# Optimization experiments

Measured on AMD Instinct MI355X. Metric: run time of the kernel, lower is better.

The kernel has to match this reference:

```python
import jax, jax.numpy as jnp
import numpy as np

B, IN, H, OUT, E = 8192, 1024, 4096, 1024, 8
HG = H // 2  # gating hidden

def setup_inputs() -> dict:
    key = jax.random.key(0)
    ks = jax.random.split(key, 9)
    s_in = 1.0 / np.sqrt(IN)
    s_h = 1.0 / np.sqrt(H)
    s_hg = 1.0 / np.sqrt(HG)
    return {
        "x": jax.random.normal(ks[0], (B, IN), jnp.float32),
        # gating MLP: Linear(IN,HG) -> ReLU -> Linear(HG,E) -> softmax
        "gw1": jax.random.uniform(ks[1], (IN, HG), jnp.float32, -s_in, s_in),
        "gb1": jax.random.uniform(ks[2], (HG,), jnp.float32, -s_in, s_in),
        "gw2": jax.random.uniform(ks[3], (HG, E), jnp.float32, -s_hg, s_hg),
        "gb2": jax.random.uniform(ks[4], (E,), jnp.float32, -s_hg, s_hg),
        # experts: E x (Linear(IN,H) -> ReLU -> Linear(H,OUT))
        "ew1": jax.random.uniform(ks[5], (E, IN, H), jnp.float32, -s_in, s_in),
        "eb1": jax.random.uniform(ks[6], (E, H), jnp.float32, -s_in, s_in),
        "ew2": jax.random.uniform(ks[7], (E, H, OUT), jnp.float32, -s_h, s_h),
        "eb2": jax.random.uniform(ks[8], (E, OUT), jnp.float32, -s_h, s_h),
    }

def reference(x, gw1, gb1, gw2, gb2, ew1, eb1, ew2, eb2):
    # Gating network (dropout is a no-op in eval)
    gh = jax.nn.relu(x @ gw1 + gb1)                       # [B, HG]
    gates = jax.nn.softmax(gh @ gw2 + gb2, axis=1)        # [B, E]
    # All experts run on the full batch
    h = jax.nn.relu(jnp.einsum('bi,eih->beh', x, ew1) + eb1[None])  # [B, E, H]
    eo = jnp.einsum('beh,eho->beo', h, ew2) + eb2[None]             # [B, E, OUT]
    # Gate-weighted combine: (stacked * gates[...,None]).sum(dim=1)
    combined = jnp.einsum('beo,be->bo', eo, gates)        # [B, OUT]
    return combined
```

## Files before the change

kernel.cpp:

```cpp
#include <hip/hip_runtime.h>


#define DI __device__ __forceinline__

typedef _Float16 f16;
typedef _Float16 f16x8 __attribute__((ext_vector_type(8)));
typedef float f32x4 __attribute__((ext_vector_type(4)));

constexpr int BSZ  = 8192;
constexpr int IND  = 1024;
constexpr int HID  = 4096;
constexpr int OUTD = 1024;
constexpr int NE   = 8;
constexpr int HGD  = 2048;

__global__ __launch_bounds__(256) void conv_f32_f16_kernel(
    const float* __restrict__ in, f16* __restrict__ out)
{
    size_t i = ((size_t)blockIdx.x * 256 + threadIdx.x) * 8;
    const float4* p = (const float4*)(in + i);
    float4 a = p[0], b = p[1];
    f16x8 v = {(f16)a.x, (f16)a.y, (f16)a.z, (f16)a.w,
               (f16)b.x, (f16)b.y, (f16)b.z, (f16)b.w};
    *(f16x8*)(out + i) = v;
}

__global__ __launch_bounds__(256) void transpose_f32_f16_kernel(
    const float* __restrict__ W, f16* __restrict__ Wt, int K, int N,
    int ldo, size_t zstride, int kostep)
{
    const int z = blockIdx.z;
    W += (size_t)z * K * N;
    f16* base = Wt + (size_t)z * zstride + (size_t)z * kostep;
    __shared__ float t[64][65];
    int n0 = blockIdx.x * 64, k0 = blockIdx.y * 64;
    int tx = threadIdx.x & 63, ty = threadIdx.x >> 6;
#pragma unroll
    for (int i = 0; i < 16; i++) {
        int k = i * 4 + ty;
        t[k][tx] = W[(size_t)(k0 + k) * N + n0 + tx];
    }
    __syncthreads();
#pragma unroll
    for (int i = 0; i < 16; i++) {
        int n = i * 4 + ty;
        base[(size_t)(n0 + n) * ldo + k0 + tx] = (f16)t[tx][n];
    }
}

DI void gload_lds16(const void* g, void* l)
{
    typedef const __attribute__((address_space(1))) unsigned int as1_t;
    typedef __attribute__((address_space(3))) unsigned int as3_t;
    __builtin_amdgcn_global_load_lds(
        (as1_t*)(unsigned long long)(__SIZE_TYPE__)g,
        (as3_t*)(unsigned int)(__SIZE_TYPE__)l,
        16, 0, 0);
}

#define SYNC_HEAD    __builtin_amdgcn_s_barrier();
#define SYNC_TAIL                                                              \
    __builtin_amdgcn_sched_barrier(0);                                         \
    __builtin_amdgcn_s_barrier();                                              \
    asm volatile("" ::: "memory");

template <bool RELU, bool GSCALE>
__global__ __launch_bounds__(512, 2) void gemm256_kernel(
    const f16* __restrict__ A, const f16* __restrict__ Bt,
    const float* __restrict__ bias, const float* __restrict__ gate,
    f16* __restrict__ Cptr, int M, int N, int K, int ldc, int e0)
{
    constexpr int BM = 256, BN = 256, BK = 64;
    constexpr int AT = BM * BK * 2, BT = BN * BK * 2;
    __shared__ __align__(16) f16 sA[2][BM * BK];
    __shared__ __align__(16) f16 sB[2][BN * BK];
    const char* sAc = (const char*)sA;
    const char* sBc = (const char*)sB;

    const int z = blockIdx.z;
    Bt   += (size_t)z * N * K;
    bias += (size_t)z * N;

    const int tid = threadIdx.x, wid = tid >> 6, lane = tid & 63;
    const int wm = wid >> 2, wn = wid & 3;
    const int nwg = gridDim.x, bid = blockIdx.x;
    const int wg = (bid & 7) * (nwg >> 3) + (bid >> 3);
    const int gx = N / BN;
    const size_t bm = (size_t)(wg / gx) * BM;
    const size_t bn = (size_t)(wg % gx) * BN;

    f32x4 acc[8][4] = {};

    const int rho  = tid >> 3;
    const int slot = (((tid & 7) << 4) ^ (((tid >> 3) & 7) << 4));
    const f16* pA = A  + (bm + rho) * (size_t)K + (slot >> 1);
    const f16* pB = Bt + (bn + rho) * (size_t)K + (slot >> 1);

    auto stA = [&](int b, int q, int T) {
        gload_lds16(pA + ((size_t)q * 64) * K + (size_t)T * BK,
                    (char*)sAc + b * AT + q * 8192 + wid * 1024);
    };
    auto stB = [&](int b, int q, int T) {
        gload_lds16(pB + ((size_t)q * 64) * K + (size_t)T * BK,
                    (char*)sBc + b * BT + q * 8192 + wid * 1024);
    };

    int offA0[8], offB0[4];
#pragma unroll
    for (int f = 0; f < 8; f++) {
        int r = wm * 128 + f * 16 + (lane & 15);
        offA0[f] = r * 128 + ((((lane >> 4) << 4)) ^ ((r & 7) << 4));
    }
#pragma unroll
    for (int f = 0; f < 4; f++) {
        int r = wn * 64 + f * 16 + (lane & 15);
        offB0[f] = r * 128 + ((((lane >> 4) << 4)) ^ ((r & 7) << 4));
    }

    f16x8 av[4][2], bv0[2][2], bv1[2][2];

#define LDAQ(B, MH)                                                            \
    _Pragma("unroll") for (int f = 0; f < 4; f++)                              \
    _Pragma("unroll") for (int kc = 0; kc < 2; kc++)                           \
        av[f][kc] = *(const f16x8*)(sAc + (B) * AT + (offA0[(MH)*4+f] ^ (kc << 6)));
#define LDBH(B, NH, BV)                                                        \
    _Pragma("unroll") for (int f = 0; f < 2; f++)                              \
    _Pragma("unroll") for (int kc = 0; kc < 2; kc++)                           \
        BV[f][kc] = *(const f16x8*)(sBc + (B) * BT + (offB0[(NH)*2+f] ^ (kc << 6)));
#define QUAD(MH, NH, BV)                                                       \
    __builtin_amdgcn_s_setprio(1);                                             \
    _Pragma("unroll") for (int f = 0; f < 4; f++)                              \
    _Pragma("unroll") for (int g = 0; g < 2; g++)                              \
    _Pragma("unroll") for (int kc = 0; kc < 2; kc++)                           \
        acc[(MH)*4+f][(NH)*2+g] = __builtin_amdgcn_mfma_f32_16x16x32_f16(      \
            av[f][kc], BV[g][kc], acc[(MH)*4+f][(NH)*2+g], 0, 0, 0);           \
    __builtin_amdgcn_s_setprio(0);

    const int NT = K / BK, NI = NT / 2;

    stA(0,0,0); stA(0,2,0); stB(0,0,0); stB(0,1,0); stB(0,2,0); stB(0,3,0);
    stA(0,1,0); stA(0,3,0);
    stA(1,0,1); stA(1,2,1); stB(1,0,1); stB(1,1,1); stB(1,2,1); stB(1,3,1);
    asm volatile("s_waitcnt vmcnt(6)");
    __builtin_amdgcn_s_barrier();
    asm volatile("" ::: "memory");

    for (int i = 0; i < NI - 1; ++i) {
        const int t = 2 * i;
        LDAQ(0, 0) LDBH(0, 0, bv0) LDBH(0, 1, bv1)
        stA(1, 1, t + 1); stA(1, 3, t + 1);
        SYNC_HEAD
        QUAD(0, 0, bv0)
        SYNC_TAIL
        stA(0, 0, t + 2); stA(0, 2, t + 2);
        SYNC_HEAD
        QUAD(0, 1, bv1)
        LDAQ(0, 1)
        SYNC_TAIL
        stB(0, 0, t + 2); stB(0, 1, t + 2);
        SYNC_HEAD
        QUAD(1, 1, bv1)
        SYNC_TAIL
        stB(0, 2, t + 2); stB(0, 3, t + 2);
        SYNC_HEAD
        QUAD(1, 0, bv0)
        asm volatile("s_waitcnt vmcnt(6)");
        SYNC_TAIL
        LDAQ(1, 0) LDBH(1, 0, bv0) LDBH(1, 1, bv1)
        stA(0, 1, t + 2); stA(0, 3, t + 2);
        SYNC_HEAD
        QUAD(0, 0, bv0)
        SYNC_TAIL
        stA(1, 0, t + 3); stA(1, 2, t + 3);
        SYNC_HEAD
        QUAD(0, 1, bv1)
        LDAQ(1, 1)
        SYNC_TAIL
        stB(1, 0, t + 3); stB(1, 1, t + 3);
        SYNC_HEAD
        QUAD(1, 1, bv1)
        SYNC_TAIL
        stB(1, 2, t + 3); stB(1, 3, t + 3);
        SYNC_HEAD
        QUAD(1, 0, bv0)
        asm volatile("s_waitcnt vmcnt(6)");
        SYNC_TAIL
    }
    {
        LDAQ(0, 0) LDBH(0, 0, bv0) LDBH(0, 1, bv1)
        stA(1, 1, NT - 1); stA(1, 3, NT - 1);
        SYNC_HEAD
        QUAD(0, 0, bv0)
        SYNC_TAIL
        SYNC_HEAD
        QUAD(0, 1, bv1)
        LDAQ(0, 1)
        SYNC_TAIL
        SYNC_HEAD
        QUAD(1, 1, bv1)
        SYNC_TAIL
        SYNC_HEAD
        QUAD(1, 0, bv0)
        asm volatile("s_waitcnt vmcnt(0)");
        SYNC_TAIL
        LDAQ(1, 0) LDBH(1, 0, bv0) LDBH(1, 1, bv1)
        SYNC_HEAD
        QUAD(0, 0, bv0)
        SYNC_TAIL
        SYNC_HEAD
        QUAD(0, 1, bv1)
        LDAQ(1, 1)
        SYNC_TAIL
        SYNC_HEAD
        QUAD(1, 1, bv1)
        SYNC_TAIL
        SYNC_HEAD
        QUAD(1, 0, bv0)
        SYNC_TAIL
    }
#undef LDAQ
#undef LDBH
#undef QUAD

    const size_t row0 = bm + (size_t)wm * 128;
    const int col0 = (int)bn + wn * 64;
    const int c0 = lane & 15, r0 = (lane >> 4) * 4;
    f16* Cz = Cptr + (size_t)z * N;
#pragma unroll
    for (int fm = 0; fm < 8; fm++)
#pragma unroll
        for (int r = 0; r < 4; r++) {
            const size_t row = row0 + fm * 16 + r0 + r;
            float g = 1.0f;
            if constexpr (GSCALE) g = gate[row * NE + e0 + z];
#pragma unroll
            for (int n = 0; n < 4; n++) {
                const size_t col = (size_t)col0 + n * 16 + c0;
                float v = acc[fm][n][r] + bias[col];
                if constexpr (RELU) v = fmaxf(v, 0.0f);
                if constexpr (GSCALE) v *= g;
                Cz[row * (size_t)ldc + col] = (f16)v;
            }
        }
}

template <bool ACCUM, int GN>
__global__ __launch_bounds__(512, 2) void gemmO_kernel(
    const f16* __restrict__ A, const f16* __restrict__ Bt,
    const float* __restrict__ bias, const float* __restrict__ gate,
    float* __restrict__ Cptr, int M, int N, int K, int ldb, int e0)
{
    constexpr int BM = 256, BN = 128, BK = 64;
    constexpr int AT = BM * BK * 2, BT = BN * BK * 2;
    __shared__ __align__(16) f16 sA[2][BM * BK];
    __shared__ __align__(16) f16 sB[2][BN * BK];
    const char* sAc = (const char*)sA;
    const char* sBc = (const char*)sB;

    const int tid = threadIdx.x, wid = tid >> 6, lane = tid & 63;
    const int wm = wid >> 2, wn = wid & 3;
    const int nwg = gridDim.x, bid = blockIdx.x;
    const int wg = (bid & 7) * (nwg >> 3) + (bid >> 3);
    const int gx = N / BN;
    const size_t bm = (size_t)(wg / gx) * BM;
    const size_t bn = (size_t)(wg % gx) * BN;

    f32x4 acc[8][2] = {};

    const int rho  = tid >> 3;
    const int slot = (((tid & 7) << 4) ^ (((tid >> 3) & 7) << 4));
    const f16* pA = A  + (bm + rho) * (size_t)K   + (slot >> 1);
    const f16* pB = Bt + (bn + rho) * (size_t)ldb + (slot >> 1);

    auto stA = [&](int b, int q, int T) {
        gload_lds16(pA + ((size_t)q * 64) * K + (size_t)T * BK,
                    (char*)sAc + b * AT + q * 8192 + wid * 1024);
    };
    auto stB = [&](int b, int q, int T) {
        gload_lds16(pB + ((size_t)q * 64) * ldb + (size_t)T * BK,
                    (char*)sBc + b * BT + q * 8192 + wid * 1024);
    };

    int offA0[8], offB0[2];
#pragma unroll
    for (int f = 0; f < 8; f++) {
        int r = wm * 128 + f * 16 + (lane & 15);
        offA0[f] = r * 128 + ((((lane >> 4) << 4)) ^ ((r & 7) << 4));
    }
#pragma unroll
    for (int f = 0; f < 2; f++) {
        int r = wn * 32 + f * 16 + (lane & 15);
        offB0[f] = r * 128 + ((((lane >> 4) << 4)) ^ ((r & 7) << 4));
    }

    f16x8 av[4], bv[2][2];

#define LDA4(B, MH, KC)                                                        \
    _Pragma("unroll") for (int f = 0; f < 4; f++)                              \
        av[f] = *(const f16x8*)(sAc + (B) * AT + (offA0[(MH)*4+f] ^ ((KC) << 6)));
#define LDBA(B)                                                                \
    _Pragma("unroll") for (int f = 0; f < 2; f++)                              \
    _Pragma("unroll") for (int kc = 0; kc < 2; kc++)                           \
        bv[f][kc] = *(const f16x8*)(sBc + (B) * BT + (offB0[f] ^ (kc << 6)));
#define OCT(MH, KC)                                                            \
    __builtin_amdgcn_s_setprio(1);                                             \
    _Pragma("unroll") for (int f = 0; f < 4; f++)                              \
    _Pragma("unroll") for (int g = 0; g < 2; g++)                              \
        acc[(MH)*4+f][g] = __builtin_amdgcn_mfma_f32_16x16x32_f16(             \
            av[f], bv[g][KC], acc[(MH)*4+f][g], 0, 0, 0);                      \
    __builtin_amdgcn_s_setprio(0);

    const int NT = K / BK, NI = NT / 2;

    stA(0,0,0); stA(0,2,0); stB(0,0,0); stB(0,1,0); stA(0,1,0); stA(0,3,0);
    stA(1,0,1); stA(1,2,1); stB(1,0,1); stB(1,1,1);
    asm volatile("s_waitcnt vmcnt(4)");
    __builtin_amdgcn_s_barrier();
    asm volatile("" ::: "memory");

    for (int i = 0; i < NI - 1; ++i) {
        const int t = 2 * i;
        LDA4(0, 0, 0) LDBA(0)
        stA(1, 1, t + 1); stA(1, 3, t + 1);
        SYNC_HEAD
        OCT(0, 0)
        LDA4(0, 0, 1)
        SYNC_TAIL
        SYNC_HEAD
        OCT(0, 1)
        LDA4(0, 1, 0)
        SYNC_TAIL
        stA(0, 0, t + 2); stA(0, 2, t + 2);
        SYNC_HEAD
        OCT(1, 0)
        LDA4(0, 1, 1)
        SYNC_TAIL
        stB(0, 0, t + 2); stB(0, 1, t + 2);
        SYNC_HEAD
        OCT(1, 1)
        asm volatile("s_waitcnt vmcnt(4)");
        SYNC_TAIL
        LDA4(1, 0, 0) LDBA(1)
        stA(0, 1, t + 2); stA(0, 3, t + 2);
        SYNC_HEAD
        OCT(0, 0)
        LDA4(1, 0, 1)
        SYNC_TAIL
        SYNC_HEAD
        OCT(0, 1)
        LDA4(1, 1, 0)
        SYNC_TAIL
        stA(1, 0, t + 3); stA(1, 2, t + 3);
        SYNC_HEAD
        OCT(1, 0)
        LDA4(1, 1, 1)
        SYNC_TAIL
        stB(1, 0, t + 3); stB(1, 1, t + 3);
        SYNC_HEAD
        OCT(1, 1)
        asm volatile("s_waitcnt vmcnt(4)");
        SYNC_TAIL
    }
    {
        LDA4(0, 0, 0) LDBA(0)
        stA(1, 1, NT - 1); stA(1, 3, NT - 1);
        SYNC_HEAD
        OCT(0, 0)
        LDA4(0, 0, 1)
        SYNC_TAIL
        SYNC_HEAD
        OCT(0, 1)
        LDA4(0, 1, 0)
        SYNC_TAIL
        SYNC_HEAD
        OCT(1, 0)
        LDA4(0, 1, 1)
        SYNC_TAIL
        SYNC_HEAD
        OCT(1, 1)
        asm volatile("s_waitcnt vmcnt(0)");
        SYNC_TAIL
        LDA4(1, 0, 0) LDBA(1)
        SYNC_HEAD
        OCT(0, 0)
        LDA4(1, 0, 1)
        SYNC_TAIL
        SYNC_HEAD
        OCT(0, 1)
        LDA4(1, 1, 0)
        SYNC_TAIL
        SYNC_HEAD
        OCT(1, 0)
        LDA4(1, 1, 1)
        SYNC_TAIL
        SYNC_HEAD
        OCT(1, 1)
        SYNC_TAIL
    }
#undef LDA4
#undef LDBA
#undef OCT

    const size_t row0 = bm + (size_t)wm * 128;
    const int col0 = (int)bn + wn * 32;
    const int c0 = lane & 15, r0 = (lane >> 4) * 4;
#pragma unroll
    for (int fm = 0; fm < 8; fm++)
#pragma unroll
        for (int r = 0; r < 4; r++) {
            const size_t row = row0 + fm * 16 + r0 + r;
            if constexpr (GN == 0) {
                const float g = gate[row * NE];
#pragma unroll
                for (int n = 0; n < 2; n++) {
                    const size_t col = (size_t)col0 + n * 16 + c0;
                    float v = (acc[fm][n][r] + bias[col]) * g;
                    float* p = Cptr + row * (size_t)N + col;
                    *p = ACCUM ? (*p + v) : v;
                }
            } else {
                float gv[GN];
#pragma unroll
                for (int j = 0; j < GN; j++) gv[j] = gate[row * NE + e0 + j];
#pragma unroll
                for (int n = 0; n < 2; n++) {
                    const size_t col = (size_t)col0 + n * 16 + c0;
                    float bb = 0.f;
#pragma unroll
                    for (int j = 0; j < GN; j++)
                        bb = fmaf(gv[j], bias[(size_t)(e0 + j) * N + col], bb);
                    float v = acc[fm][n][r] + bb;
                    float* p = Cptr + row * (size_t)N + col;
                    *p = ACCUM ? (*p + v) : v;
                }
            }
        }
}

__global__ __launch_bounds__(256) void gate_softmax_kernel(
    const f16* __restrict__ gh, const float* __restrict__ gw2,
    const float* __restrict__ gb2, float* __restrict__ gates)
{
    const int row  = blockIdx.x * 4 + (threadIdx.x >> 6);
    const int lane = threadIdx.x & 63;
    const f16* r = gh + (size_t)row * HGD;
    float acc[NE] = {};
    for (int kb = lane * 8; kb < HGD; kb += 512) {
        f16x8 v = *(const f16x8*)(r + kb);
#pragma unroll
        for (int j = 0; j < 8; j++) {
            float h = (float)v[j];
            const float* w = gw2 + (size_t)(kb + j) * NE;
#pragma unroll
            for (int e = 0; e < NE; e++) acc[e] = fmaf(h, w[e], acc[e]);
        }
    }
#pragma unroll
    for (int off = 32; off > 0; off >>= 1)
#pragma unroll
        for (int e = 0; e < NE; e++) acc[e] += __shfl_down(acc[e], off, 64);
    if (lane == 0) {
        float l[NE], m = -1e30f;
#pragma unroll
        for (int e = 0; e < NE; e++) { l[e] = acc[e] + gb2[e]; m = fmaxf(m, l[e]); }
        float s = 0.f;
#pragma unroll
        for (int e = 0; e < NE; e++) { l[e] = expf(l[e] - m); s += l[e]; }
        float inv = 1.0f / s;
#pragma unroll
        for (int e = 0; e < NE; e++) gates[(size_t)row * NE + e] = l[e] * inv;
    }
}

extern "C" void kernel_launch(void* const* d_in, const int* in_sizes, int n_in,
                              void* d_out, int out_size, void* d_ws, size_t ws_size,
                              hipStream_t stream)
{
    const float* x   = (const float*)d_in[0];
    const float* gw1 = (const float*)d_in[1];
    const float* gb1 = (const float*)d_in[2];
    const float* gw2 = (const float*)d_in[3];
    const float* gb2 = (const float*)d_in[4];
    const float* ew1 = (const float*)d_in[5];
    const float* eb1 = (const float*)d_in[6];
    const float* ew2 = (const float*)d_in[7];
    const float* eb2 = (const float*)d_in[8];
    float* out = (float*)d_out;

    const size_t SZ_GATES = 256 << 10;
    const size_t SZ_X16   = (size_t)BSZ * IND * 2;
    const size_t SZ_WBUF  = (size_t)HID * IND * 2;
    const size_t SZ_W1ALL = (size_t)NE * HID * IND * 2;
    const size_t SZ_W2ALL = (size_t)NE * OUTD * HID * 2;
    const size_t SZ_HB1   = (size_t)BSZ * HID * 2;
    const size_t BASE     = SZ_GATES + SZ_X16 + SZ_W1ALL + SZ_W2ALL;
    const size_t NEED_G4  = BASE + 4 * SZ_HB1;
    const size_t NEED_G2  = BASE + 2 * SZ_HB1;
    const size_t NEED_G1  = BASE + 1 * SZ_HB1;

    char* p = (char*)d_ws;
    float* gates = (float*)p;  p += SZ_GATES;
    f16* x16 = (f16*)p;        p += SZ_X16;

    conv_f32_f16_kernel<<<(BSZ * IND) / (256 * 8), 256, 0, stream>>>(x, x16);

    if (ws_size >= NEED_G2) {
        const int G = (ws_size >= NEED_G4) ? 4 : 2;
        f16* w1all = (f16*)p;  p += SZ_W1ALL;
        f16* w2cat = (f16*)p;  p += SZ_W2ALL;
        f16* hbufG = (f16*)p;
        f16* gh    = hbufG;

        transpose_f32_f16_kernel<<<dim3(HGD / 64, IND / 64, 1), 256, 0, stream>>>(
            gw1, w1all, IND, HGD, IND, 0, 0);
        gemm256_kernel<true, false>
            <<<dim3((HGD / 256) * (BSZ / 256), 1, 1), 512, 0, stream>>>(
                x16, w1all, gb1, nullptr, gh, BSZ, HGD, IND, HGD, 0);
        gate_softmax_kernel<<<BSZ / 4, 256, 0, stream>>>(gh, gw2, gb2, gates);

        transpose_f32_f16_kernel<<<dim3(HID / 64, IND / 64, NE), 256, 0, stream>>>(
            ew1, w1all, IND, HID, IND, (size_t)HID * IND, 0);
        transpose_f32_f16_kernel<<<dim3(OUTD / 64, HID / 64, NE), 256, 0, stream>>>(
            ew2, w2cat, HID, OUTD, NE * HID, 0, HID);

        for (int g = 0; g < NE / G; g++) {
            gemm256_kernel<true, true>
                <<<dim3((HID / 256) * (BSZ / 256), 1, G), 512, 0, stream>>>(
                    x16, w1all + (size_t)g * G * HID * IND, eb1 + g * G * HID,
                    gates, hbufG, BSZ, HID, IND, G * HID, g * G);
            if (G == 4) {
                if (g == 0)
                    gemmO_kernel<false, 4>
                        <<<(OUTD / 128) * (BSZ / 256), 512, 0, stream>>>(
                            hbufG, w2cat + (size_t)g * G * HID, eb2, gates, out,
                            BSZ, OUTD, G * HID, NE * HID, g * G);
                else
                    gemmO_kernel<true, 4>
                        <<<(OUTD / 128) * (BSZ / 256), 512, 0, stream>>>(
                            hbufG, w2cat + (size_t)g * G * HID, eb2, gates, out,
                            BSZ, OUTD, G * HID, NE * HID, g * G);
            } else {
                if (g == 0)
                    gemmO_kernel<false, 2>
                        <<<(OUTD / 128) * (BSZ / 256), 512, 0, stream>>>(
                            hbufG, w2cat + (size_t)g * G * HID, eb2, gates, out,
                            BSZ, OUTD, G * HID, NE * HID, g * G);
                else
                    gemmO_kernel<true, 2>
                        <<<(OUTD / 128) * (BSZ / 256), 512, 0, stream>>>(
                            hbufG, w2cat + (size_t)g * G * HID, eb2, gates, out,
                            BSZ, OUTD, G * HID, NE * HID, g * G);
            }
        }
    } else if (ws_size >= NEED_G1) {
        f16* w1all = (f16*)p;  p += SZ_W1ALL;
        f16* w2all = (f16*)p;  p += SZ_W2ALL;
        f16* hbuf  = (f16*)p;
        f16* gh    = hbuf;

        transpose_f32_f16_kernel<<<dim3(HGD / 64, IND / 64, 1), 256, 0, stream>>>(
            gw1, w1all, IND, HGD, IND, 0, 0);
        gemm256_kernel<true, false>
            <<<dim3((HGD / 256) * (BSZ / 256), 1, 1), 512, 0, stream>>>(
                x16, w1all, gb1, nullptr, gh, BSZ, HGD, IND, HGD, 0);
        gate_softmax_kernel<<<BSZ / 4, 256, 0, stream>>>(gh, gw2, gb2, gates);

        transpose_f32_f16_kernel<<<dim3(HID / 64, IND / 64, NE), 256, 0, stream>>>(
            ew1, w1all, IND, HID, IND, (size_t)HID * IND, 0);
        transpose_f32_f16_kernel<<<dim3(OUTD / 64, HID / 64, NE), 256, 0, stream>>>(
            ew2, w2all, HID, OUTD, HID, (size_t)OUTD * HID, 0);

        for (int e = 0; e < NE; e++) {
            gemm256_kernel<true, false>
                <<<dim3((HID / 256) * (BSZ / 256), 1, 1), 512, 0, stream>>>(
                    x16, w1all + (size_t)e * HID * IND, eb1 + (size_t)e * HID,
                    nullptr, hbuf, BSZ, HID, IND, HID, 0);
            if (e == 0)
                gemmO_kernel<false, 0><<<(OUTD / 128) * (BSZ / 256), 512, 0, stream>>>(
                    hbuf, w2all + (size_t)e * OUTD * HID, eb2 + (size_t)e * OUTD,
                    gates + e, out, BSZ, OUTD, HID, HID, 0);
            else
                gemmO_kernel<true, 0><<<(OUTD / 128) * (BSZ / 256), 512, 0, stream>>>(
                    hbuf, w2all + (size_t)e * OUTD * HID, eb2 + (size_t)e * OUTD,
                    gates + e, out, BSZ, OUTD, HID, HID, 0);
        }
    } else {
        f16* wbuf = (f16*)p;   p += SZ_WBUF;
        f16* hbuf = (f16*)p;
        f16* gh   = hbuf;

        transpose_f32_f16_kernel<<<dim3(HGD / 64, IND / 64, 1), 256, 0, stream>>>(
            gw1, wbuf, IND, HGD, IND, 0, 0);
        gemm256_kernel<true, false>
            <<<dim3((HGD / 256) * (BSZ / 256), 1, 1), 512, 0, stream>>>(
                x16, wbuf, gb1, nullptr, gh, BSZ, HGD, IND, HGD, 0);
        gate_softmax_kernel<<<BSZ / 4, 256, 0, stream>>>(gh, gw2, gb2, gates);

        for (int e = 0; e < NE; e++) {
            transpose_f32_f16_kernel<<<dim3(HID / 64, IND / 64, 1), 256, 0, stream>>>(
                ew1 + (size_t)e * IND * HID, wbuf, IND, HID, IND, 0, 0);
            gemm256_kernel<true, false>
                <<<dim3((HID / 256) * (BSZ / 256), 1, 1), 512, 0, stream>>>(
                    x16, wbuf, eb1 + (size_t)e * HID, nullptr, hbuf,
                    BSZ, HID, IND, HID, 0);

            transpose_f32_f16_kernel<<<dim3(OUTD / 64, HID / 64, 1), 256, 0, stream>>>(
                ew2 + (size_t)e * HID * OUTD, wbuf, HID, OUTD, HID, 0, 0);
            if (e == 0)
                gemmO_kernel<false, 0><<<(OUTD / 128) * (BSZ / 256), 512, 0, stream>>>(
                    hbuf, wbuf, eb2 + (size_t)e * OUTD, gates + e, out,
                    BSZ, OUTD, HID, HID, 0);
            else
                gemmO_kernel<true, 0><<<(OUTD / 128) * (BSZ / 256), 512, 0, stream>>>(
                    hbuf, wbuf, eb2 + (size_t)e * OUTD, gates + e, out,
                    BSZ, OUTD, HID, HID, 0);
        }
    }
}
```

Baseline: 1.309 ms.

## Restructure GEMM main loops into two barrier phases per K-tile

Both GEMM kernels' software pipelines are rewritten so each K-tile is processed in two larger phases (one per M-half) instead of four or eight smaller ones. Each phase covers all N fragments, which halves the number of block barriers per tile. Global-to-LDS stage issues are regrouped, and the vmcnt waits are set to the new outstanding-load counts with an explicit drain at the tail. Fewer barriers cut synchronisation overhead and give the scheduler longer MFMA runs. The cost is more registers for the A fragments and less fine-grained interleaving of loads with compute.

New measurement: 1.338 ms. +2.2%, slower.

```diff
diff --git a/kernel.cpp b/kernel.cpp
--- a/kernel.cpp
+++ b/kernel.cpp
@@ -63,6 +63,12 @@
     __builtin_amdgcn_sched_barrier(0);                                         \
     __builtin_amdgcn_s_barrier();                                              \
     asm volatile("" ::: "memory");
+
+#define VM8 asm volatile("s_waitcnt vmcnt(8)");
+#define VM6 asm volatile("s_waitcnt vmcnt(6)");
+#define VM4 asm volatile("s_waitcnt vmcnt(4)");
+#define VM2 asm volatile("s_waitcnt vmcnt(2)");
+#define VM0 asm volatile("s_waitcnt vmcnt(0)");
 
 template <bool RELU, bool GSCALE>
 __global__ __launch_bounds__(512, 2) void gemm256_kernel(
@@ -127,100 +133,54 @@
     _Pragma("unroll") for (int f = 0; f < 2; f++)                              \
     _Pragma("unroll") for (int kc = 0; kc < 2; kc++)                           \
         BV[f][kc] = *(const f16x8*)(sBc + (B) * BT + (offB0[(NH)*2+f] ^ (kc << 6)));
-#define QUAD(MH, NH, BV)                                                       \
+#define MFMA_MH(MH)                                                            \
     __builtin_amdgcn_s_setprio(1);                                             \
     _Pragma("unroll") for (int f = 0; f < 4; f++)                              \
     _Pragma("unroll") for (int g = 0; g < 2; g++)                              \
-    _Pragma("unroll") for (int kc = 0; kc < 2; kc++)                           \
-        acc[(MH)*4+f][(NH)*2+g] = __builtin_amdgcn_mfma_f32_16x16x32_f16(      \
-            av[f][kc], BV[g][kc], acc[(MH)*4+f][(NH)*2+g], 0, 0, 0);           \
+    _Pragma("unroll") for (int kc = 0; kc < 2; kc++) {                         \
+        acc[(MH)*4+f][g]   = __builtin_amdgcn_mfma_f32_16x16x32_f16(           \
+            av[f][kc], bv0[g][kc], acc[(MH)*4+f][g],   0, 0, 0);               \
+        acc[(MH)*4+f][2+g] = __builtin_amdgcn_mfma_f32_16x16x32_f16(           \
+            av[f][kc], bv1[g][kc], acc[(MH)*4+f][2+g], 0, 0, 0);               \
+    }                                                                          \
     __builtin_amdgcn_s_setprio(0);
 
-    const int NT = K / BK, NI = NT / 2;
+#define TILE_A(B, STAGE, VM)                                                   \
+  { LDAQ(B, 0) LDBH(B, 0, bv0) LDBH(B, 1, bv1)                                 \
+    STAGE                                                                      \
+    SYNC_HEAD MFMA_MH(0) VM SYNC_TAIL }
+#define TILE_B(B, STAGE, VM)                                                   \
+  { LDAQ(B, 1)                                                                 \
+    STAGE                                                                      \
+    SYNC_HEAD MFMA_MH(1) VM SYNC_TAIL }
+
+    const int NT = K / BK;
 
     stA(0,0,0); stA(0,2,0); stB(0,0,0); stB(0,1,0); stB(0,2,0); stB(0,3,0);
     stA(0,1,0); stA(0,3,0);
     stA(1,0,1); stA(1,2,1); stB(1,0,1); stB(1,1,1); stB(1,2,1); stB(1,3,1);
-    asm volatile("s_waitcnt vmcnt(6)");
+    VM6
     __builtin_amdgcn_s_barrier();
     asm volatile("" ::: "memory");
 
-    for (int i = 0; i < NI - 1; ++i) {
-        const int t = 2 * i;
-        LDAQ(0, 0) LDBH(0, 0, bv0) LDBH(0, 1, bv1)
-        stA(1, 1, t + 1); stA(1, 3, t + 1);
-        SYNC_HEAD
-        QUAD(0, 0, bv0)
-        SYNC_TAIL
-        stA(0, 0, t + 2); stA(0, 2, t + 2);
-        SYNC_HEAD
-        QUAD(0, 1, bv1)
-        LDAQ(0, 1)
-        SYNC_TAIL
-        stB(0, 0, t + 2); stB(0, 1, t + 2);
-        SYNC_HEAD
-        QUAD(1, 1, bv1)
-        SYNC_TAIL
-        stB(0, 2, t + 2); stB(0, 3, t + 2);
-        SYNC_HEAD
-        QUAD(1, 0, bv0)
-        asm volatile("s_waitcnt vmcnt(6)");
-        SYNC_TAIL
-        LDAQ(1, 0) LDBH(1, 0, bv0) LDBH(1, 1, bv1)
-        stA(0, 1, t + 2); stA(0, 3, t + 2);
-        SYNC_HEAD
-        QUAD(0, 0, bv0)
-        SYNC_TAIL
-        stA(1, 0, t + 3); stA(1, 2, t + 3);
-        SYNC_HEAD
-        QUAD(0, 1, bv1)
-        LDAQ(1, 1)
-        SYNC_TAIL
-        stB(1, 0, t + 3); stB(1, 1, t + 3);
-        SYNC_HEAD
-        QUAD(1, 1, bv1)
-        SYNC_TAIL
-        stB(1, 2, t + 3); stB(1, 3, t + 3);
-        SYNC_HEAD
-        QUAD(1, 0, bv0)
-        asm volatile("s_waitcnt vmcnt(6)");
-        SYNC_TAIL
-    }
-    {
-        LDAQ(0, 0) LDBH(0, 0, bv0) LDBH(0, 1, bv1)
-        stA(1, 1, NT - 1); stA(1, 3, NT - 1);
-        SYNC_HEAD
-        QUAD(0, 0, bv0)
-        SYNC_TAIL
-        SYNC_HEAD
-        QUAD(0, 1, bv1)
-        LDAQ(0, 1)
-        SYNC_TAIL
-        SYNC_HEAD
-        QUAD(1, 1, bv1)
-        SYNC_TAIL
-        SYNC_HEAD
-        QUAD(1, 0, bv0)
-        asm volatile("s_waitcnt vmcnt(0)");
-        SYNC_TAIL
-        LDAQ(1, 0) LDBH(1, 0, bv0) LDBH(1, 1, bv1)
-        SYNC_HEAD
-        QUAD(0, 0, bv0)
-        SYNC_TAIL
-        SYNC_HEAD
-        QUAD(0, 1, bv1)
-        LDAQ(1, 1)
-        SYNC_TAIL
-        SYNC_HEAD
-        QUAD(1, 1, bv1)
-        SYNC_TAIL
-        SYNC_HEAD
-        QUAD(1, 0, bv0)
-        SYNC_TAIL
-    }
+    for (int t = 0; t < NT - 2; t += 2) {
+        TILE_A(0, { stA(1,1,t+1); stA(1,3,t+1); }, VM8)
+        TILE_B(0, { stA(0,0,t+2); stA(0,2,t+2);
+                    stB(0,0,t+2); stB(0,1,t+2); stB(0,2,t+2); stB(0,3,t+2); }, VM8)
+        TILE_A(1, { stA(0,1,t+2); stA(0,3,t+2); }, VM8)
+        TILE_B(1, { stA(1,0,t+3); stA(1,2,t+3);
+                    stB(1,0,t+3); stB(1,1,t+3); stB(1,2,t+3); stB(1,3,t+3); }, VM8)
+    }
+    TILE_A(0, { stA(1,1,NT-1); stA(1,3,NT-1); }, VM8)
+    TILE_B(0, {}, VM2)
+    TILE_A(1, {}, VM0)
+    TILE_B(1, {}, )
+
 #undef LDAQ
 #undef LDBH
-#undef QUAD
+#undef MFMA_MH
+#undef TILE_A
+#undef TILE_B
 
     const size_t row0 = bm + (size_t)wm * 128;
     const int col0 = (int)bn + wn * 64;
@@ -293,113 +253,59 @@
         offB0[f] = r * 128 + ((((lane >> 4) << 4)) ^ ((r & 7) << 4));
     }
 
-    f16x8 av[4], bv[2][2];
-
-#define LDA4(B, MH, KC)                                                        \
+    f16x8 av[4][2], bv[2][2];
+
+#define LDAO(B, MH)                                                            \
     _Pragma("unroll") for (int f = 0; f < 4; f++)                              \
-        av[f] = *(const f16x8*)(sAc + (B) * AT + (offA0[(MH)*4+f] ^ ((KC) << 6)));
+    _Pragma("unroll") for (int kc = 0; kc < 2; kc++)                           \
+        av[f][kc] = *(const f16x8*)(sAc + (B) * AT + (offA0[(MH)*4+f] ^ (kc << 6)));
 #define LDBA(B)                                                                \
     _Pragma("unroll") for (int f = 0; f < 2; f++)                              \
     _Pragma("unroll") for (int kc = 0; kc < 2; kc++)                           \
         bv[f][kc] = *(const f16x8*)(sBc + (B) * BT + (offB0[f] ^ (kc << 6)));
-#define OCT(MH, KC)                                                            \
+#define MFMAO(MH)                                                              \
     __builtin_amdgcn_s_setprio(1);                                             \
     _Pragma("unroll") for (int f = 0; f < 4; f++)                              \
     _Pragma("unroll") for (int g = 0; g < 2; g++)                              \
+    _Pragma("unroll") for (int kc = 0; kc < 2; kc++)                           \
         acc[(MH)*4+f][g] = __builtin_amdgcn_mfma_f32_16x16x32_f16(             \
-            av[f], bv[g][KC], acc[(MH)*4+f][g], 0, 0, 0);                      \
+            av[f][kc], bv[g][kc], acc[(MH)*4+f][g], 0, 0, 0);                  \
     __builtin_amdgcn_s_setprio(0);
 
-    const int NT = K / BK, NI = NT / 2;
-
-    stA(0,0,0); stA(0,2,0); stB(0,0,0); stB(0,1,0); stA(0,1,0); stA(0,3,0);
+#define TO_A(B, STAGE, VM)                                                     \
+  { LDAO(B, 0) LDBA(B)                                                         \
+    STAGE                                                                      \
+    SYNC_HEAD MFMAO(0) VM SYNC_TAIL }
+#define TO_B(B, STAGE, VM)                                                     \
+  { LDAO(B, 1)                                                                 \
+    STAGE                                                                      \
+    SYNC_HEAD MFMAO(1) VM SYNC_TAIL }
+
+    const int NT = K / BK;
+
+    stA(0,0,0); stA(0,2,0); stB(0,0,0); stB(0,1,0);
+    stA(0,1,0); stA(0,3,0);
     stA(1,0,1); stA(1,2,1); stB(1,0,1); stB(1,1,1);
-    asm volatile("s_waitcnt vmcnt(4)");
+    VM4
     __builtin_amdgcn_s_barrier();
     asm volatile("" ::: "memory");
 
-    for (int i = 0; i < NI - 1; ++i) {
-        const int t = 2 * i;
-        LDA4(0, 0, 0) LDBA(0)
-        stA(1, 1, t + 1); stA(1, 3, t + 1);
-        SYNC_HEAD
-        OCT(0, 0)
-        LDA4(0, 0, 1)
-        SYNC_TAIL
-        SYNC_HEAD
-        OCT(0, 1)
-        LDA4(0, 1, 0)
-        SYNC_TAIL
-        stA(0, 0, t + 2); stA(0, 2, t + 2);
-        SYNC_HEAD
-        OCT(1, 0)
-        LDA4(0, 1, 1)
-        SYNC_TAIL
-        stB(0, 0, t + 2); stB(0, 1, t + 2);
-        SYNC_HEAD
-        OCT(1, 1)
-        asm volatile("s_waitcnt vmcnt(4)");
-        SYNC_TAIL
-        LDA4(1, 0, 0) LDBA(1)
-        stA(0, 1, t + 2); stA(0, 3, t + 2);
-        SYNC_HEAD
-        OCT(0, 0)
-        LDA4(1, 0, 1)
-        SYNC_TAIL
-        SYNC_HEAD
-        OCT(0, 1)
-        LDA4(1, 1, 0)
-        SYNC_TAIL
-        stA(1, 0, t + 3); stA(1, 2, t + 3);
-        SYNC_HEAD
-        OCT(1, 0)
-        LDA4(1, 1, 1)
-        SYNC_TAIL
-        stB(1, 0, t + 3); stB(1, 1, t + 3);
-        SYNC_HEAD
-        OCT(1, 1)
-        asm volatile("s_waitcnt vmcnt(4)");
-        SYNC_TAIL
-    }
-    {
-        LDA4(0, 0, 0) LDBA(0)
-        stA(1, 1, NT - 1); stA(1, 3, NT - 1);
-        SYNC_HEAD
-        OCT(0, 0)
-        LDA4(0, 0, 1)
-        SYNC_TAIL
-        SYNC_HEAD
-        OCT(0, 1)
-        LDA4(0, 1, 0)
-        SYNC_TAIL
-        SYNC_HEAD
-        OCT(1, 0)
-        LDA4(0, 1, 1)
-        SYNC_TAIL
-        SYNC_HEAD
-        OCT(1, 1)
-        asm volatile("s_waitcnt vmcnt(0)");
-        SYNC_TAIL
-        LDA4(1, 0, 0) LDBA(1)
-        SYNC_HEAD
-        OCT(0, 0)
-        LDA4(1, 0, 1)
-        SYNC_TAIL
-        SYNC_HEAD
-        OCT(0, 1)
-        LDA4(1, 1, 0)
-        SYNC_TAIL
-        SYNC_HEAD
-        OCT(1, 0)
-        LDA4(1, 1, 1)
-        SYNC_TAIL
-        SYNC_HEAD
-        OCT(1, 1)
-        SYNC_TAIL
-    }
-#undef LDA4
+    for (int t = 0; t < NT - 2; t += 2) {
+        TO_A(0, { stA(1,1,t+1); stA(1,3,t+1); }, VM6)
+        TO_B(0, { stA(0,0,t+2); stA(0,2,t+2); stB(0,0,t+2); stB(0,1,t+2); }, VM6)
+        TO_A(1, { stA(0,1,t+2); stA(0,3,t+2); }, VM6)
+        TO_B(1, { stA(1,0,t+3); stA(1,2,t+3); stB(1,0,t+3); stB(1,1,t+3); }, VM6)
+    }
+    TO_A(0, { stA(1,1,NT-1); stA(1,3,NT-1); }, VM6)
+    TO_B(0, {}, VM2)
+    TO_A(1, {}, VM0)
+    TO_B(1, {}, )
+
+#undef LDAO
 #undef LDBA
-#undef OCT
+#undef MFMAO
+#undef TO_A
+#undef TO_B
 
     const size_t row0 = bm + (size_t)wm * 128;
     const int col0 = (int)bn + wn * 32;
```
